# Performance work log

Hardware: AMD Instinct MI355X
Metric: run time of the kernel (lower is better)

Reference implementation:

```python
import jax, jax.numpy as jnp
import numpy as np

N, E, D_IN, D_H, G = 50000, 800000, 300, 128, 128


def gat_conv(x, src, dst, W, att_src, att_dst, bias):
    # PyG GATConv, heads=1, concat, negative_slope=0.2, self-loops already appended.
    h = x @ W                              # [N, F]
    a_s = h @ att_src                      # [N]
    a_d = h @ att_dst                      # [N]
    e = jax.nn.leaky_relu(a_s[src] + a_d[dst], 0.2)   # [E+N]
    m = jax.ops.segment_max(e, dst, num_segments=h.shape[0])
    ex = jnp.exp(e - m[dst])
    denom = jax.ops.segment_sum(ex, dst, num_segments=h.shape[0])
    alpha = ex / denom[dst]                # softmax over in-edges of each dst
    out = jax.ops.segment_sum(alpha[:, None] * h[src], dst, num_segments=h.shape[0])
    return out + bias


def setup_inputs() -> dict:
    key = jax.random.key(0)
    ks = jax.random.split(key, 12)
    x = jax.random.normal(ks[0], (N, D_IN), dtype=jnp.float32)
    edge_index = jax.random.randint(ks[1], (2, E), 0, N)
    batch = jnp.sort(jax.random.randint(ks[2], (N,), 0, G))
    pos = jax.random.randint(ks[3], (N,), 0, 2).astype(bool)
    s = 0.05
    W1 = jax.random.normal(ks[4], (D_IN, D_H), dtype=jnp.float32) * s
    as1 = jax.random.normal(ks[5], (D_H,), dtype=jnp.float32) * s
    ad1 = jax.random.normal(ks[6], (D_H,), dtype=jnp.float32) * s
    b1 = jnp.zeros((D_H,), dtype=jnp.float32)
    W2 = jax.random.normal(ks[7], (D_H, D_H), dtype=jnp.float32) * s
    as2 = jax.random.normal(ks[8], (D_H,), dtype=jnp.float32) * s
    ad2 = jax.random.normal(ks[9], (D_H,), dtype=jnp.float32) * s
    b2 = jnp.zeros((D_H,), dtype=jnp.float32)
    Wfc = jax.random.normal(ks[10], (D_H, 1), dtype=jnp.float32) * s
    bfc = jnp.zeros((1,), dtype=jnp.float32)
    return {"x": x, "edge_index": edge_index, "batch": batch, "pos": pos,
            "num_graphs": G, "W1": W1, "as1": as1, "ad1": ad1, "b1": b1,
            "W2": W2, "as2": as2, "ad2": ad2, "b2": b2, "Wfc": Wfc, "bfc": bfc}


def reference(x, edge_index, batch, pos, num_graphs, W1, as1, ad1, b1,
              W2, as2, ad2, b2, Wfc, bfc):
    n = x.shape[0]
    loop = jnp.arange(n)
    src = jnp.concatenate([edge_index[0], loop])
    dst = jnp.concatenate([edge_index[1], loop])
    h = gat_conv(x, src, dst, W1, as1, ad1, b1)
    h = jax.nn.gelu(h, approximate=False)
    # dropout is identity in eval mode
    h = gat_conv(h, src, dst, W2, as2, ad2, b2)   # [N, 128]
    # masked per-graph mean: logits[g] = mean over nodes with batch==g and pos
    w = pos.astype(h.dtype)                       # [N]
    sums = jax.ops.segment_sum(h * w[:, None], batch, num_segments=num_graphs)
    cnt = jax.ops.segment_sum(w, batch, num_segments=num_graphs)
    logits = sums / jnp.maximum(cnt, 1.0)[:, None]          # [G, 128]
    scores = (jax.nn.gelu(logits, approximate=False) @ Wfc + bfc).reshape(-1, num_graphs)
    return scores, logits
```

## Files before the change

### kernel.cpp

```cpp
#include <hip/hip_runtime.h>
#include <math.h>

#define NN 50000
#define EE 800000
#define DIN 300
#define DH 128
#define NG 128
#define LDA 40

typedef __attribute__((ext_vector_type(8))) short short8;
typedef __attribute__((ext_vector_type(4))) float floatx4;

__device__ __forceinline__ float gelu_exact(float x) {
  return 0.5f * x * (1.0f + erff(x * 0.7071067811865476f));
}

__device__ __forceinline__ void split_bf16(float v, unsigned short& hi, unsigned short& lo) {
  unsigned int u = __float_as_uint(v);
  hi = (unsigned short)(u >> 16);
  float fh = __uint_as_float((unsigned int)hi << 16);
  lo = (unsigned short)(__float_as_uint(v - fh) >> 16);
}

__device__ __forceinline__ unsigned short f2bf_rne(float x) {
  unsigned int u = __float_as_uint(x);
  unsigned int r = (u + 0x7FFFu + ((u >> 16) & 1u)) >> 16;
  return (unsigned short)r;
}

__device__ __forceinline__ float bf_lo(unsigned u) { return __uint_as_float(u << 16); }
__device__ __forceinline__ float bf_hi(unsigned u) { return __uint_as_float(u & 0xFFFF0000u); }


__global__ __launch_bounds__(256) void count_deg_kernel(const int* __restrict__ ei,
                                                        int* __restrict__ deg) {
  int e = blockIdx.x * 256 + threadIdx.x;
  if (e >= EE + NN) return;
  int d = (e < EE) ? ei[EE + e] : (e - EE);
  atomicAdd(&deg[d], 1);
}

__global__ __launch_bounds__(1024) void scan_part_kernel(const int* __restrict__ deg,
                                                         int* __restrict__ rowptr,
                                                         int* __restrict__ bsum) {
  __shared__ int wsum[16];
  const int tid = threadIdx.x;
  const int lane = tid & 63;
  const int wid = tid >> 6;
  int idx = blockIdx.x * 1024 + tid;
  int v = (idx < NN) ? deg[idx] : 0;
  int x = v;
#pragma unroll
  for (int d = 1; d < 64; d <<= 1) {
    int y = __shfl_up(x, d, 64);
    if (lane >= d) x += y;
  }
  if (lane == 63) wsum[wid] = x;
  __syncthreads();
  if (wid == 0) {
    int s = (lane < 16) ? wsum[lane] : 0;
#pragma unroll
    for (int d = 1; d < 16; d <<= 1) {
      int y = __shfl_up(s, d, 64);
      if (lane >= d) s += y;
    }
    if (lane < 16) wsum[lane] = s;
  }
  __syncthreads();
  int woff = (wid > 0) ? wsum[wid - 1] : 0;
  int incl = x + woff;
  if (idx < NN) rowptr[idx] = incl - v;
  if (tid == 1023) bsum[blockIdx.x] = incl;
}

__global__ __launch_bounds__(64) void scan_sums_kernel(const int* __restrict__ bsum,
                                                       int* __restrict__ boff, int nb) {
  int lane = threadIdx.x;
  int v = (lane < nb) ? bsum[lane] : 0;
  int x = v;
#pragma unroll
  for (int d = 1; d < 64; d <<= 1) {
    int y = __shfl_up(x, d, 64);
    if (lane >= d) x += y;
  }
  if (lane < nb) boff[lane] = x - v;
  if (lane == nb - 1) boff[nb] = x;
}

__global__ __launch_bounds__(256) void scan_add_kernel(int* __restrict__ rowptr,
                                                       const int* __restrict__ boff,
                                                       int* __restrict__ cursor, int nb) {
  int i = blockIdx.x * 256 + threadIdx.x;
  if (i < NN) {
    int r = rowptr[i] + boff[i >> 10];
    rowptr[i] = r;
    cursor[i] = r;
  } else if (i == NN) {
    rowptr[NN] = boff[nb];
  }
}

__global__ __launch_bounds__(256) void scatter_kernel(const int* __restrict__ ei,
                                                      int* __restrict__ cursor,
                                                      int* __restrict__ colA) {
  int e = blockIdx.x * 256 + threadIdx.x;
  if (e >= EE + NN) return;
  int s, d;
  if (e < EE) { s = ei[e]; d = ei[EE + e]; }
  else        { s = e - EE; d = e - EE; }
  int p = atomicAdd(&cursor[d], 1);
  colA[p] = s;
}


__global__ __launch_bounds__(256) void convert_bt_kernel(const float* __restrict__ B,
                                                         unsigned short* __restrict__ Bth,
                                                         unsigned short* __restrict__ Btl,
                                                         int K, int Kpad) {
  int i = blockIdx.x * 256 + threadIdx.x;
  int n = i / Kpad, k = i % Kpad;
  if (n >= 128) return;
  float v = (k < K) ? B[(long)k * 128 + n] : 0.f;
  unsigned short h, l;
  split_bf16(v, h, l);
  Bth[(long)n * Kpad + k] = h;
  Btl[(long)n * Kpad + k] = l;
}


__global__ __launch_bounds__(256) void gemm_mfma_kernel(
    const float* __restrict__ A,
    const unsigned short* __restrict__ Bth, const unsigned short* __restrict__ Btl,
    unsigned short* __restrict__ C, int M, int K, int Kpad,
    const float* __restrict__ avs, const float* __restrict__ avd,
    float* __restrict__ aS, float* __restrict__ aD) {
  __shared__ unsigned short Ah[64 * LDA];
  __shared__ unsigned short Al[64 * LDA];
  __shared__ unsigned short Bh[128 * LDA];
  __shared__ unsigned short Bl[128 * LDA];

  const int tid = threadIdx.x;
  const int lane = tid & 63;
  const int w = tid >> 6;
  const int wr = w >> 1, wc = w & 1;
  const int q = lane >> 4;
  const int m16 = lane & 15;
  const int row0 = blockIdx.x * 64;

  floatx4 acc[2][4];
#pragma unroll
  for (int i = 0; i < 2; i++)
#pragma unroll
    for (int j = 0; j < 4; j++) acc[i][j] = (floatx4)(0.f);

  const int nsteps = Kpad / 32;
  for (int s = 0; s < nsteps; s++) {
    const int k0 = s * 32;
#pragma unroll
    for (int p = 0; p < 2; p++) {
      int e = p * 256 + tid;
      int r = e >> 3;
      int q4 = e & 7;
      int gr = row0 + r, gk = k0 + q4 * 4;
      float4 v = make_float4(0.f, 0.f, 0.f, 0.f);
      if (gr < M && gk < K) v = *(const float4*)&A[(long)gr * K + gk];
      unsigned short h0, h1, h2, h3, l0, l1, l2, l3;
      split_bf16(v.x, h0, l0);
      split_bf16(v.y, h1, l1);
      split_bf16(v.z, h2, l2);
      split_bf16(v.w, h3, l3);
      uint2 hh, ll;
      hh.x = (unsigned)h0 | ((unsigned)h1 << 16);
      hh.y = (unsigned)h2 | ((unsigned)h3 << 16);
      ll.x = (unsigned)l0 | ((unsigned)l1 << 16);
      ll.y = (unsigned)l2 | ((unsigned)l3 << 16);
      *(uint2*)&Ah[r * LDA + q4 * 4] = hh;
      *(uint2*)&Al[r * LDA + q4 * 4] = ll;
    }
#pragma unroll
    for (int p = 0; p < 2; p++) {
      int e = p * 256 + tid;
      int n = e & 127;
      int sel = e >> 7;
      const unsigned short* src = (sel & 2) ? Btl : Bth;
      unsigned short* dst = (sel & 2) ? Bl : Bh;
      int kk = (sel & 1) * 16;
      uint4 v0 = *(const uint4*)&src[(long)n * Kpad + k0 + kk];
      uint4 v1 = *(const uint4*)&src[(long)n * Kpad + k0 + kk + 8];
      *(uint4*)&dst[n * LDA + kk] = v0;
      *(uint4*)&dst[n * LDA + kk + 8] = v1;
    }
    __syncthreads();
    short8 afh[2], afl[2];
#pragma unroll
    for (int rt = 0; rt < 2; rt++) {
      int r = wr * 32 + rt * 16 + m16;
      afh[rt] = *(const short8*)&Ah[r * LDA + q * 8];
      afl[rt] = *(const short8*)&Al[r * LDA + q * 8];
    }
#pragma unroll
    for (int ct = 0; ct < 4; ct++) {
      int n = wc * 64 + ct * 16 + m16;
      short8 bfh = *(const short8*)&Bh[n * LDA + q * 8];
      short8 bfl = *(const short8*)&Bl[n * LDA + q * 8];
#pragma unroll
      for (int rt = 0; rt < 2; rt++) {
        acc[rt][ct] = __builtin_amdgcn_mfma_f32_16x16x32_bf16(afh[rt], bfh, acc[rt][ct], 0, 0, 0);
        acc[rt][ct] = __builtin_amdgcn_mfma_f32_16x16x32_bf16(afh[rt], bfl, acc[rt][ct], 0, 0, 0);
        acc[rt][ct] = __builtin_amdgcn_mfma_f32_16x16x32_bf16(afl[rt], bfh, acc[rt][ct], 0, 0, 0);
      }
    }
    __syncthreads();
  }

  float avs_r[4], avd_r[4];
#pragma unroll
  for (int ct = 0; ct < 4; ct++) {
    int n = wc * 64 + ct * 16 + m16;
    avs_r[ct] = avs[n];
    avd_r[ct] = avd[n];
  }
#pragma unroll
  for (int rt = 0; rt < 2; rt++) {
    int rbase = row0 + wr * 32 + rt * 16 + q * 4;
#pragma unroll
    for (int reg = 0; reg < 4; reg++) {
      int grow = rbase + reg;
      bool ok = grow < M;
      float ps = 0.f, pd = 0.f;
#pragma unroll
      for (int ct = 0; ct < 4; ct++) {
        float c = acc[rt][ct][reg];
        if (ok) C[(long)grow * 128 + wc * 64 + ct * 16 + m16] = f2bf_rne(c);
        ps = fmaf(c, avs_r[ct], ps);
        pd = fmaf(c, avd_r[ct], pd);
      }
#pragma unroll
      for (int d = 1; d < 16; d <<= 1) {
        ps += __shfl_xor(ps, d, 64);
        pd += __shfl_xor(pd, d, 64);
      }
      if (m16 == 0 && ok) {
        atomicAdd(&aS[grow], ps);
        atomicAdd(&aD[grow], pd);
      }
    }
  }
}


__global__ __launch_bounds__(256) void aggregate_kernel(const int* __restrict__ rowptr,
                                                        const int* __restrict__ colA,
                                                        const float* __restrict__ aS,
                                                        const float* __restrict__ aD,
                                                        const unsigned short* __restrict__ Hb,
                                                        const float* __restrict__ bias,
                                                        float* __restrict__ out,
                                                        int apply_gelu) {
  const int lane = threadIdx.x & 63;
  const int dst = blockIdx.x * 4 + (threadIdx.x >> 6);
  if (dst >= NN) return;
  const int start = rowptr[dst];
  const int end = rowptr[dst + 1];
  const int deg = end - start;
  const float ad = aD[dst];
  const int half = lane >> 5;
  const int fl = lane & 31;

  float a0 = 0.f, a1 = 0.f, a2 = 0.f, a3 = 0.f;

  if (deg <= 64) {
    int src = 0;
    float e = -__builtin_inff();
    if (lane < deg) {
      src = colA[start + lane];
      float v = aS[src] + ad;
      e = (v > 0.f) ? v : 0.2f * v;
    }
    float mx = e;
#pragma unroll
    for (int d = 1; d < 64; d <<= 1) mx = fmaxf(mx, __shfl_xor(mx, d, 64));
    float ew = (lane < deg) ? expf(e - mx) : 0.f;
    float ss = ew;
#pragma unroll
    for (int d = 1; d < 64; d <<= 1) ss += __shfl_xor(ss, d, 64);
    float wgt = ew * (1.f / ss);
    for (int j = 0; j < deg; j += 4) {
      int j0 = j + half;
      int j1 = j + 2 + half;
      int sj0 = __shfl(src, j0, 64);
      float wj0 = __shfl(wgt, j0, 64);
      int sj1 = __shfl(src, j1, 64);
      float wj1 = __shfl(wgt, j1, 64);
      uint2 u0 = *(const uint2*)&Hb[(long)sj0 * DH + fl * 4];
      uint2 u1 = *(const uint2*)&Hb[(long)sj1 * DH + fl * 4];
      a0 = fmaf(wj0, bf_lo(u0.x), a0);
      a1 = fmaf(wj0, bf_hi(u0.x), a1);
      a2 = fmaf(wj0, bf_lo(u0.y), a2);
      a3 = fmaf(wj0, bf_hi(u0.y), a3);
      a0 = fmaf(wj1, bf_lo(u1.x), a0);
      a1 = fmaf(wj1, bf_hi(u1.x), a1);
      a2 = fmaf(wj1, bf_lo(u1.y), a2);
      a3 = fmaf(wj1, bf_hi(u1.y), a3);
    }
  } else {
    float m = -__builtin_inff(), ssum = 0.f;
    for (int c0 = start; c0 < end; c0 += 64) {
      int i = c0 + lane;
      float e = -__builtin_inff();
      if (i < end) {
        int s = colA[i];
        float v = aS[s] + ad;
        e = (v > 0.f) ? v : 0.2f * v;
      }
      float cm = e;
#pragma unroll
      for (int d = 1; d < 64; d <<= 1) cm = fmaxf(cm, __shfl_xor(cm, d, 64));
      float ce = (i < end) ? expf(e - cm) : 0.f;
      float cs = ce;
#pragma unroll
      for (int d = 1; d < 64; d <<= 1) cs += __shfl_xor(cs, d, 64);
      float nm = fmaxf(m, cm);
      ssum = ssum * expf(m - nm) + cs * expf(cm - nm);
      m = nm;
    }
    float inv = 1.f / ssum;
    for (int c0 = start; c0 < end; c0 += 64) {
      int i = c0 + lane;
      int src = 0;
      float wgt = 0.f;
      if (i < end) {
        src = colA[i];
        float v = aS[src] + ad;
        float e = (v > 0.f) ? v : 0.2f * v;
        wgt = expf(e - m) * inv;
      }
      int lim = min(64, end - c0);
      for (int j = 0; j < lim; j += 4) {
        int j0 = j + half;
        int j1 = j + 2 + half;
        int sj0 = __shfl(src, j0, 64);
        float wj0 = __shfl(wgt, j0, 64);
        int sj1 = __shfl(src, j1, 64);
        float wj1 = __shfl(wgt, j1, 64);
        uint2 u0 = *(const uint2*)&Hb[(long)sj0 * DH + fl * 4];
        uint2 u1 = *(const uint2*)&Hb[(long)sj1 * DH + fl * 4];
        a0 = fmaf(wj0, bf_lo(u0.x), a0);
        a1 = fmaf(wj0, bf_hi(u0.x), a1);
        a2 = fmaf(wj0, bf_lo(u0.y), a2);
        a3 = fmaf(wj0, bf_hi(u0.y), a3);
        a0 = fmaf(wj1, bf_lo(u1.x), a0);
        a1 = fmaf(wj1, bf_hi(u1.x), a1);
        a2 = fmaf(wj1, bf_lo(u1.y), a2);
        a3 = fmaf(wj1, bf_hi(u1.y), a3);
      }
    }
  }

  a0 += __shfl_xor(a0, 32, 64);
  a1 += __shfl_xor(a1, 32, 64);
  a2 += __shfl_xor(a2, 32, 64);
  a3 += __shfl_xor(a3, 32, 64);

  if (half == 0) {
    float4 b = *(const float4*)&bias[fl * 4];
    float r0 = a0 + b.x;
    float r1 = a1 + b.y;
    float r2 = a2 + b.z;
    float r3 = a3 + b.w;
    if (apply_gelu) {
      r0 = gelu_exact(r0); r1 = gelu_exact(r1);
      r2 = gelu_exact(r2); r3 = gelu_exact(r3);
    }
    *(float4*)&out[(long)dst * DH + fl * 4] = make_float4(r0, r1, r2, r3);
  }
}


__global__ __launch_bounds__(128) void pool_kernel(const float* __restrict__ H,
                                                   const int* __restrict__ batch,
                                                   const int* __restrict__ pos,
                                                   float* __restrict__ sums,
                                                   float* __restrict__ cnt) {
  const int CH = 64;
  int n0 = blockIdx.x * CH;
  int n1 = min(n0 + CH, NN);
  int f = threadIdx.x;
  float acc = 0.f, c = 0.f;
  int g = batch[n0];
  for (int n = n0; n < n1; n++) {
    int gn = batch[n];
    if (gn != g) {
      atomicAdd(&sums[g * DH + f], acc);
      if (f == 0) atomicAdd(&cnt[g], c);
      acc = 0.f; c = 0.f; g = gn;
    }
    if (pos[n]) {
      acc += H[(long)n * DH + f];
      c += 1.f;
    }
  }
  atomicAdd(&sums[g * DH + f], acc);
  if (f == 0) atomicAdd(&cnt[g], c);
}


__global__ __launch_bounds__(128) void head_kernel(const float* __restrict__ sums,
                                                   const float* __restrict__ cnt,
                                                   const float* __restrict__ Wfc,
                                                   const float* __restrict__ bfc,
                                                   float* __restrict__ out) {
  int g = blockIdx.x;
  int f = threadIdx.x;
  float c = fmaxf(cnt[g], 1.f);
  float logit = sums[g * DH + f] / c;
  out[NG + g * DH + f] = logit;
  float gl = gelu_exact(logit) * Wfc[f];
  __shared__ float red[2];
#pragma unroll
  for (int d = 1; d < 64; d <<= 1) gl += __shfl_xor(gl, d, 64);
  int lane = f & 63, w = f >> 6;
  if (lane == 0) red[w] = gl;
  __syncthreads();
  if (f == 0) out[g] = red[0] + red[1] + bfc[0];
}


extern "C" void kernel_launch(void* const* d_in, const int* in_sizes, int n_in,
                              void* d_out, int out_size, void* d_ws, size_t ws_size,
                              hipStream_t stream) {
  const float* x   = (const float*)d_in[0];
  const int* ei    = (const int*)d_in[1];
  const int* batch = (const int*)d_in[2];
  const int* pos   = (const int*)d_in[3];
  const float* W1  = (const float*)d_in[5];
  const float* as1 = (const float*)d_in[6];
  const float* ad1 = (const float*)d_in[7];
  const float* b1  = (const float*)d_in[8];
  const float* W2  = (const float*)d_in[9];
  const float* as2 = (const float*)d_in[10];
  const float* ad2 = (const float*)d_in[11];
  const float* b2  = (const float*)d_in[12];
  const float* Wfc = (const float*)d_in[13];
  const float* bfc = (const float*)d_in[14];
  float* out = (float*)d_out;

  const int KP1 = 320;
  const int KP2 = 128;
  const int NB_SCAN = (NN + 1023) / 1024;

  char* ws = (char*)d_ws;
  size_t off = 0;
  auto nxt = [&](size_t b) -> void* {
    size_t p = off;
    off += (b + 255) & ~(size_t)255;
    return (void*)(ws + p);
  };
  int* rowptr = (int*)nxt((NN + 1) * sizeof(int));
  int* cursor = (int*)nxt(NN * sizeof(int));
  int* colA   = (int*)nxt((size_t)(EE + NN) * sizeof(int));
  int* bsum   = (int*)nxt((NB_SCAN + 1) * sizeof(int));
  int* boff   = (int*)nxt((NB_SCAN + 1) * sizeof(int));
  float* aS   = (float*)nxt((size_t)2 * NN * sizeof(float));
  float* aD   = aS + NN;
  unsigned short* bufAb = (unsigned short*)nxt((size_t)NN * DH * sizeof(short));
  float* bufB = (float*)nxt((size_t)NN * DH * sizeof(float));
  float* sums = (float*)nxt((size_t)(NG * DH + NG) * sizeof(float));
  float* cnt  = sums + NG * DH;
  unsigned short* Bt1h = (unsigned short*)nxt((size_t)128 * KP1 * sizeof(short));
  unsigned short* Bt1l = (unsigned short*)nxt((size_t)128 * KP1 * sizeof(short));
  unsigned short* Bt2h = (unsigned short*)nxt((size_t)128 * KP2 * sizeof(short));
  unsigned short* Bt2l = (unsigned short*)nxt((size_t)128 * KP2 * sizeof(short));

  hipMemsetAsync(cursor, 0, NN * sizeof(int), stream);
  hipMemsetAsync(sums, 0, (NG * DH + NG) * sizeof(float), stream);
  hipMemsetAsync(aS, 0, (size_t)2 * NN * sizeof(float), stream);

  convert_bt_kernel<<<(128 * KP1 + 255) / 256, 256, 0, stream>>>(W1, Bt1h, Bt1l, DIN, KP1);
  convert_bt_kernel<<<(128 * KP2 + 255) / 256, 256, 0, stream>>>(W2, Bt2h, Bt2l, DH, KP2);

  const int eb = (EE + NN + 255) / 256;
  count_deg_kernel<<<eb, 256, 0, stream>>>(ei, cursor);
  scan_part_kernel<<<NB_SCAN, 1024, 0, stream>>>(cursor, rowptr, bsum);
  scan_sums_kernel<<<1, 64, 0, stream>>>(bsum, boff, NB_SCAN);
  scan_add_kernel<<<(NN + 1 + 255) / 256, 256, 0, stream>>>(rowptr, boff, cursor, NB_SCAN);
  scatter_kernel<<<eb, 256, 0, stream>>>(ei, cursor, colA);

  const int gblocks = (NN + 63) / 64;
  gemm_mfma_kernel<<<gblocks, 256, 0, stream>>>(x, Bt1h, Bt1l, bufAb, NN, DIN, KP1,
                                                as1, ad1, aS, aD);
  aggregate_kernel<<<(NN + 3) / 4, 256, 0, stream>>>(rowptr, colA, aS, aD, bufAb, b1, bufB, 1);
  hipMemsetAsync(aS, 0, (size_t)2 * NN * sizeof(float), stream);
  gemm_mfma_kernel<<<gblocks, 256, 0, stream>>>(bufB, Bt2h, Bt2l, bufAb, NN, DH, KP2,
                                                as2, ad2, aS, aD);
  aggregate_kernel<<<(NN + 3) / 4, 256, 0, stream>>>(rowptr, colA, aS, aD, bufAb, b2, bufB, 0);
  pool_kernel<<<(NN + 63) / 64, 128, 0, stream>>>(bufB, batch, pos, sums, cnt);
  head_kernel<<<NG, 128, 0, stream>>>(sums, cnt, Wfc, bfc, out);
}
```

Before: 375.7 us.

## Partition CSR build atomics by destination range per XCD

Count-degree and scatter kernels now assign each block to one of 8 destination-node ranges (selected by block index mod 8), with blocks grid-striding over all edges and only processing edges whose destination falls in their range. The intent is to localize atomic traffic on the degree/cursor arrays to one XCD's L2 and reduce cross-die contention. In exchange each edge's destination is read 8 times and most threads skip work, raising read traffic.

```diff
diff --git a/kernel.cpp b/kernel.cpp
--- a/kernel.cpp
+++ b/kernel.cpp
@@ -7,6 +7,7 @@
 #define DH 128
 #define NG 128
 #define LDA 40
+#define RSIZE 6250
 
 typedef __attribute__((ext_vector_type(8))) short short8;
 typedef __attribute__((ext_vector_type(4))) float floatx4;
@@ -32,12 +33,21 @@
 __device__ __forceinline__ float bf_hi(unsigned u) { return __uint_as_float(u & 0xFFFF0000u); }
 
 
-__global__ __launch_bounds__(256) void count_deg_kernel(const int* __restrict__ ei,
-                                                        int* __restrict__ deg) {
-  int e = blockIdx.x * 256 + threadIdx.x;
-  if (e >= EE + NN) return;
-  int d = (e < EE) ? ei[EE + e] : (e - EE);
-  atomicAdd(&deg[d], 1);
+__global__ __launch_bounds__(256) void count_part_kernel(const int* __restrict__ ei,
+                                                         int* __restrict__ deg,
+                                                         int blocksPerRange) {
+  const int r = blockIdx.x & 7;
+  const int t = blockIdx.x >> 3;
+  const int lo = r * RSIZE, hi = lo + RSIZE;
+  const int total = EE + NN;
+  const int step = blocksPerRange * 256;
+  for (int e0 = t * 256; e0 < total; e0 += step) {
+    int e = e0 + threadIdx.x;
+    if (e < total) {
+      int d = (e < EE) ? ei[EE + e] : (e - EE);
+      if (d >= lo && d < hi) atomicAdd(&deg[d], 1);
+    }
+  }
 }
 
 __global__ __launch_bounds__(1024) void scan_part_kernel(const int* __restrict__ deg,
@@ -100,16 +110,26 @@
   }
 }
 
-__global__ __launch_bounds__(256) void scatter_kernel(const int* __restrict__ ei,
-                                                      int* __restrict__ cursor,
-                                                      int* __restrict__ colA) {
-  int e = blockIdx.x * 256 + threadIdx.x;
-  if (e >= EE + NN) return;
-  int s, d;
-  if (e < EE) { s = ei[e]; d = ei[EE + e]; }
-  else        { s = e - EE; d = e - EE; }
-  int p = atomicAdd(&cursor[d], 1);
-  colA[p] = s;
+__global__ __launch_bounds__(256) void scatter_part_kernel(const int* __restrict__ ei,
+                                                           int* __restrict__ cursor,
+                                                           int* __restrict__ colA,
+                                                           int blocksPerRange) {
+  const int r = blockIdx.x & 7;
+  const int t = blockIdx.x >> 3;
+  const int lo = r * RSIZE, hi = lo + RSIZE;
+  const int total = EE + NN;
+  const int step = blocksPerRange * 256;
+  for (int e0 = t * 256; e0 < total; e0 += step) {
+    int e = e0 + threadIdx.x;
+    if (e < total) {
+      int d = (e < EE) ? ei[EE + e] : (e - EE);
+      if (d >= lo && d < hi) {
+        int s = (e < EE) ? ei[e] : d;
+        int p = atomicAdd(&cursor[d], 1);
+        colA[p] = s;
+      }
+    }
+  }
 }
 
 
@@ -448,6 +468,7 @@
   const int KP1 = 320;
   const int KP2 = 128;
   const int NB_SCAN = (NN + 1023) / 1024;
+  const int BPR = 416;
 
   char* ws = (char*)d_ws;
   size_t off = 0;
@@ -479,12 +500,11 @@
   convert_bt_kernel<<<(128 * KP1 + 255) / 256, 256, 0, stream>>>(W1, Bt1h, Bt1l, DIN, KP1);
   convert_bt_kernel<<<(128 * KP2 + 255) / 256, 256, 0, stream>>>(W2, Bt2h, Bt2l, DH, KP2);
 
-  const int eb = (EE + NN + 255) / 256;
-  count_deg_kernel<<<eb, 256, 0, stream>>>(ei, cursor);
+  count_part_kernel<<<8 * BPR, 256, 0, stream>>>(ei, cursor, BPR);
   scan_part_kernel<<<NB_SCAN, 1024, 0, stream>>>(cursor, rowptr, bsum);
   scan_sums_kernel<<<1, 64, 0, stream>>>(bsum, boff, NB_SCAN);
   scan_add_kernel<<<(NN + 1 + 255) / 256, 256, 0, stream>>>(rowptr, boff, cursor, NB_SCAN);
-  scatter_kernel<<<eb, 256, 0, stream>>>(ei, cursor, colA);
+  scatter_part_kernel<<<8 * BPR, 256, 0, stream>>>(ei, cursor, colA, BPR);
 
   const int gblocks = (NN + 63) / 64;
   gemm_mfma_kernel<<<gblocks, 256, 0, stream>>>(x, Bt1h, Bt1l, bufAb, NN, DIN, KP1,
```

Measured after the change: 366.4 us. 2.5% less time.
